# Kernel optimization log

Measured on AMD Instinct MI355X. Metric: run time of the kernel, lower is better.

Reference implementation:

```python
import jax, jax.numpy as jnp
import numpy as np

S = 8192        # packed patch tokens
D = 1024        # hidden_size
H = 16          # num_heads
DH = D // H     # head_dim = 64
N_SEG = 8       # images
SEG = S // N_SEG


def _rope_tables(seq_len, dim, theta=10000.0):
    inv_freq = 1.0 / (theta ** (jnp.arange(0, dim, 2, dtype=jnp.float32) / dim))
    pos = jnp.arange(seq_len, dtype=jnp.float32)
    freqs = pos[:, None] * inv_freq[None, :]          # [S, dim//2]
    emb = jnp.concatenate([freqs, freqs], axis=-1)    # [S, dim]
    return jnp.cos(emb), jnp.sin(emb)


def setup_inputs() -> dict:
    key = jax.random.key(0)
    ks = jax.random.split(key, 6)
    hidden_states = jax.random.normal(ks[0], (S, D), dtype=jnp.float32)
    cu_seqlens = (jnp.arange(N_SEG + 1, dtype=jnp.int32) * SEG)
    cos, sin = _rope_tables(S, DH)
    scale = 1.0 / np.sqrt(D)
    qkv_w = jax.random.normal(ks[1], (3 * D, D), dtype=jnp.float32) * scale
    qkv_b = jax.random.normal(ks[2], (3 * D,), dtype=jnp.float32) * 0.02
    proj_w = jax.random.normal(ks[3], (D, D), dtype=jnp.float32) * scale
    proj_b = jax.random.normal(ks[4], (D,), dtype=jnp.float32) * 0.02
    return {"hidden_states": hidden_states, "cos": cos, "sin": sin,
            "qkv_w": qkv_w, "qkv_b": qkv_b, "proj_w": proj_w, "proj_b": proj_b,
            "cu_seqlens": cu_seqlens}


def _rotate_half(x):
    x1, x2 = jnp.split(x, 2, axis=-1)
    return jnp.concatenate([-x2, x1], axis=-1)


def reference(hidden_states, cos, sin, qkv_w, qkv_b, proj_w, proj_b, cu_seqlens):
    seq = hidden_states.shape[0]
    n_seg = cu_seqlens.shape[0] - 1
    seg = seq // n_seg  # equal-length packed segments

    qkv = hidden_states @ qkv_w.T + qkv_b                # [S, 3D]
    qkv = qkv.reshape(seq, 3, H, DH)
    q, k, v = qkv[:, 0], qkv[:, 1], qkv[:, 2]            # [S, H, DH]

    # rotary in fp32, cos/sin broadcast over heads (unsqueeze(-2))
    cosf = cos[:, None, :].astype(jnp.float32)
    sinf = sin[:, None, :].astype(jnp.float32)
    qf = q.astype(jnp.float32)
    kf = k.astype(jnp.float32)
    q = (qf * cosf + _rotate_half(qf) * sinf).astype(q.dtype)
    k = (kf * cosf + _rotate_half(kf) * sinf).astype(k.dtype)

    # block-diagonal attention over cu_seqlens segments (all equal length)
    qb = q.reshape(n_seg, seg, H, DH)
    kb = k.reshape(n_seg, seg, H, DH)
    vb = v.reshape(n_seg, seg, H, DH)
    scaling = DH ** -0.5
    scores = jnp.einsum('nqhd,nkhd->nhqk', qb, kb) * scaling
    probs = jax.nn.softmax(scores.astype(jnp.float32), axis=-1).astype(qb.dtype)
    out = jnp.einsum('nhqk,nkhd->nqhd', probs, vb)       # [n, seg, H, DH]
    out = out.reshape(seq, D)

    return out @ proj_w.T + proj_b
```

## Files before the change

kernel.cpp:

```cpp
#include <hip/hip_runtime.h>
#include <hip/hip_bf16.h>
#include <cstdint>
#include <cstddef>

typedef __bf16 bf16_t;
typedef __bf16 bf16x4 __attribute__((ext_vector_type(4)));
typedef __bf16 bf16x8 __attribute__((ext_vector_type(8)));
typedef float  f32x4  __attribute__((ext_vector_type(4)));

#define S_LEN 8192
#define NHEAD 16
#define DHEAD 64
#define NSEG  8
#define SEG   1024

#define QSCALE 0.1803368801111204f

__device__ __forceinline__ void stage16(const void* gsrc, void* lds_base, int lane) {
#if __has_builtin(__builtin_amdgcn_global_load_lds)
  (void)lane;
  __builtin_amdgcn_global_load_lds(
      (__attribute__((address_space(1))) void*)(gsrc),
      (__attribute__((address_space(3))) void*)(lds_base), 16, 0, 0);
#else
  ((uint4*)lds_base)[lane] = *(const uint4*)gsrc;
#endif
}

__global__ __launch_bounds__(256) void cvt_tile_kernel(
    const float* __restrict__ s0, bf16_t* __restrict__ d0,
    const float* __restrict__ s1, bf16_t* __restrict__ d1,
    const float* __restrict__ s2, bf16_t* __restrict__ d2) {
  __shared__ __align__(16) bf16_t T[16 * 1024];
  int b = blockIdx.x;
  const float* src; bf16_t* dst; int rb;
  if (b < 512)      { src = s0; dst = d0; rb = b; }
  else if (b < 704) { src = s1; dst = d1; rb = b - 512; }
  else              { src = s2; dst = d2; rb = b - 704; }
  const int t = threadIdx.x;
  const size_t base4 = (size_t)rb * 4096;
#pragma unroll
  for (int i = 0; i < 16; i++) {
    int f = i * 256 + t;
    float4 v = ((const float4*)src)[base4 + f];
    bf16x4 o = {(bf16_t)v.x, (bf16_t)v.y, (bf16_t)v.z, (bf16_t)v.w};
    *(bf16x4*)&T[f * 4] = o;
  }
  __syncthreads();
  bf16_t* dt = dst + (size_t)rb * 16384;
#pragma unroll
  for (int i = 0; i < 8; i++) {
    int o = i * 2048 + t * 8;
    int tile = o >> 9, kb = (o >> 7) & 3, r = (o >> 3) & 15;
    bf16x8 v = *(const bf16x8*)&T[r * 1024 + tile * 32 + kb * 8];
    *(bf16x8*)&dt[o] = v;
  }
}

template<int MODE, int N, int K>
__global__ __launch_bounds__(256, 2) void gemm_bt_kernel(
    const bf16_t* __restrict__ A, const bf16_t* __restrict__ B,
    const float* __restrict__ bias, void* __restrict__ Cout,
    bf16_t* __restrict__ vt, const float* __restrict__ cosT,
    const float* __restrict__ sinT) {
  __shared__ __align__(16) bf16_t As[2][128 * 32];
  __shared__ __align__(16) bf16_t Bs[2][128 * 32];
  const int tid = threadIdx.x;
  const int wv = tid >> 6, lane = tid & 63;
  const int quad = lane >> 4, l16 = lane & 15;
  const int m0 = blockIdx.y * 128, n0 = blockIdx.x * 128;
  const int wm = (wv >> 1) * 64, wn = (wv & 1) * 64;

  constexpr int KT = K / 32;
  const int c0 = wv * 2, c1 = wv * 2 + 1;
  const bf16_t* Ap0 = A + ((size_t)((m0 >> 4) + c0) * KT) * 512 + lane * 8;
  const bf16_t* Ap1 = A + ((size_t)((m0 >> 4) + c1) * KT) * 512 + lane * 8;
  const bf16_t* Bp0 = B + ((size_t)((n0 >> 4) + c0) * KT) * 512 + lane * 8;
  const bf16_t* Bp1 = B + ((size_t)((n0 >> 4) + c1) * KT) * 512 + lane * 8;

  f32x4 acc[4][4];
#pragma unroll
  for (int i = 0; i < 4; i++)
#pragma unroll
    for (int j = 0; j < 4; j++) {
      f32x4 z = {0.f, 0.f, 0.f, 0.f};
      acc[i][j] = z;
    }

  stage16(Ap0, &As[0][c0 * 512], lane);
  stage16(Ap1, &As[0][c1 * 512], lane);
  stage16(Bp0, &Bs[0][c0 * 512], lane);
  stage16(Bp1, &Bs[0][c1 * 512], lane);

  for (int kbi = 0; kbi < KT; kbi++) {
    __syncthreads();
    if (kbi + 1 < KT) {
      const int kb = (kbi + 1) * 512;
      bf16_t* ad = As[(kbi + 1) & 1];
      bf16_t* bd = Bs[(kbi + 1) & 1];
      stage16(Ap0 + kb, ad + c0 * 512, lane);
      stage16(Ap1 + kb, ad + c1 * 512, lane);
      stage16(Bp0 + kb, bd + c0 * 512, lane);
      stage16(Bp1 + kb, bd + c1 * 512, lane);
    }
    const bf16_t* as = As[kbi & 1];
    const bf16_t* bs = Bs[kbi & 1];
    bf16x8 af[4], bfr[4];
#pragma unroll
    for (int i = 0; i < 4; i++)
      af[i] = *(const bf16x8*)&as[((wm >> 4) + i) * 512 + lane * 8];
#pragma unroll
    for (int j = 0; j < 4; j++)
      bfr[j] = *(const bf16x8*)&bs[((wn >> 4) + j) * 512 + lane * 8];
#pragma unroll
    for (int i = 0; i < 4; i++)
#pragma unroll
      for (int j = 0; j < 4; j++)
        acc[i][j] = __builtin_amdgcn_mfma_f32_16x16x32_bf16(af[i], bfr[j], acc[i][j], 0, 0, 0);
  }

#pragma unroll
  for (int i = 0; i < 4; i++) {
    const int row = m0 + wm + i * 16 + quad * 4;
#pragma unroll
    for (int j = 0; j < 4; j++) {
      const int col = n0 + wn + j * 16 + l16;
      if (MODE == 0) {
        if (col < 2048) {
          if (j < 2) {
            bf16_t* qkp = (bf16_t*)Cout;
            const int d = col & 63;
            const float bv0 = bias[col];
            const float bv1 = bias[col + 32];
            const bool isq = (col < 1024);
            const int cb0 = (col >> 3) & 7;
            const int cb1 = cb0 + 4;
            const size_t base = (size_t)(col & ~63);
#pragma unroll
            for (int r = 0; r < 4; r++) {
              const int s = row + r;
              const float c = cosT[s * 64 + d];
              const float sn = sinT[s * 64 + d];
              const float x1 = acc[i][j][r] + bv0;
              const float x2 = acc[i][j + 2][r] + bv1;
              float o1 = x1 * c - x2 * sn;
              float o2 = x2 * c + x1 * sn;
              if (isq) { o1 *= QSCALE; o2 *= QSCALE; }
              const int sw = s & 7;
              const size_t rb = (size_t)s * 2048 + base + (col & 7);
              qkp[rb + ((cb0 ^ sw) * 8)] = (bf16_t)o1;
              qkp[rb + ((cb1 ^ sw) * 8)] = (bf16_t)o2;
            }
          }
        } else {
          const float bv = bias[col];
          const int h = (col - 2048) >> 6, d = (col - 2048) & 63;
          const int seg = row >> 10, kl0 = row & 1023;
          const int blk = (((kl0 & 63) >> 3) ^ (d & 7));
          bf16x4 pk = {(bf16_t)(acc[i][j][0] + bv), (bf16_t)(acc[i][j][1] + bv),
                       (bf16_t)(acc[i][j][2] + bv), (bf16_t)(acc[i][j][3] + bv)};
          *(bf16x4*)&vt[((size_t)((seg * NHEAD + h) * DHEAD + d)) * SEG +
                        (kl0 & ~63) + blk * 8 + (kl0 & 7)] = pk;
        }
      } else {
        const float bv = bias[col];
        float* cp = (float*)Cout;
#pragma unroll
        for (int r = 0; r < 4; r++)
          cp[(size_t)(row + r) * N + col] = acc[i][j][r] + bv;
      }
    }
  }
}

__global__ __launch_bounds__(256, 2) void attn_kernel(
    const bf16_t* __restrict__ qk, const bf16_t* __restrict__ vt,
    bf16_t* __restrict__ attn) {
  __shared__ __align__(16) bf16_t Qs[64 * 64];
  __shared__ __align__(16) bf16_t Ks[2][64 * 64];
  __shared__ __align__(16) bf16_t Vs[2][64 * 64];
  __shared__ __align__(16) bf16_t Ps[4][16 * 64];

  const int bid = blockIdx.x;
  const int qt = bid & 15;
  const int h = (bid >> 4) & 15;
  const int seg = bid >> 8;
  const int tid = threadIdx.x;
  const int wv = tid >> 6, lane = tid & 63;
  const int quad = lane >> 4, l16 = lane & 15;
  const int swl = l16 & 7;

  const int c0 = wv * 2, c1 = c0 + 1;
  const int r8 = lane >> 3;
  const int k8 = (lane & 7) * 8;

  const bf16_t* kbase = qk + 1024 + h * 64;
  const bf16_t* vbase = vt + (size_t)((seg * NHEAD + h) * DHEAD) * SEG;

  {
    size_t rowbase = (size_t)(seg * SEG + qt * 64);
    stage16(qk + (rowbase + c0 * 8 + r8) * 2048 + h * 64 + k8, &Qs[c0 * 512], lane);
    stage16(qk + (rowbase + c1 * 8 + r8) * 2048 + h * 64 + k8, &Qs[c1 * 512], lane);
    size_t krow = (size_t)(seg * SEG);
    stage16(kbase + (krow + c0 * 8 + r8) * 2048 + k8, &Ks[0][c0 * 512], lane);
    stage16(kbase + (krow + c1 * 8 + r8) * 2048 + k8, &Ks[0][c1 * 512], lane);
    stage16(vbase + (size_t)(c0 * 8 + r8) * SEG + k8, &Vs[0][c0 * 512], lane);
    stage16(vbase + (size_t)(c1 * 8 + r8) * SEG + k8, &Vs[0][c1 * 512], lane);
  }
  __syncthreads();
  const bf16x8 aq0 = *(const bf16x8*)&Qs[(wv * 16 + l16) * 64 + (quad ^ swl) * 8];
  const bf16x8 aq1 = *(const bf16x8*)&Qs[(wv * 16 + l16) * 64 + ((quad + 4) ^ swl) * 8];

  float rs[4] = {0.f, 0.f, 0.f, 0.f};
  f32x4 o[4];
#pragma unroll
  for (int jd = 0; jd < 4; jd++) { f32x4 z = {0.f, 0.f, 0.f, 0.f}; o[jd] = z; }

  for (int kt = 0; kt < 16; kt++) {
    __syncthreads();
    if (kt + 1 < 16) {
      const int nb = (kt + 1) & 1;
      size_t krow = (size_t)(seg * SEG + (kt + 1) * 64);
      stage16(kbase + (krow + c0 * 8 + r8) * 2048 + k8, &Ks[nb][c0 * 512], lane);
      stage16(kbase + (krow + c1 * 8 + r8) * 2048 + k8, &Ks[nb][c1 * 512], lane);
      stage16(vbase + (size_t)(c0 * 8 + r8) * SEG + (kt + 1) * 64 + k8, &Vs[nb][c0 * 512], lane);
      stage16(vbase + (size_t)(c1 * 8 + r8) * SEG + (kt + 1) * 64 + k8, &Vs[nb][c1 * 512], lane);
    }
    const bf16_t* ks = Ks[kt & 1];
    const bf16_t* vs = Vs[kt & 1];

    f32x4 sacc[4];
#pragma unroll
    for (int j = 0; j < 4; j++) {
      bf16x8 b0 = *(const bf16x8*)&ks[(j * 16 + l16) * 64 + (quad ^ swl) * 8];
      bf16x8 b1 = *(const bf16x8*)&ks[(j * 16 + l16) * 64 + ((quad + 4) ^ swl) * 8];
      f32x4 s = {0.f, 0.f, 0.f, 0.f};
      s = __builtin_amdgcn_mfma_f32_16x16x32_bf16(aq0, b0, s, 0, 0, 0);
      s = __builtin_amdgcn_mfma_f32_16x16x32_bf16(aq1, b1, s, 0, 0, 0);
      sacc[j] = s;
    }

#pragma unroll
    for (int j = 0; j < 4; j++)
#pragma unroll
      for (int r = 0; r < 4; r++) {
        float e = exp2f(sacc[j][r]);
        rs[r] += e;
        const int prow = quad * 4 + r;
        const int pblk = (j * 2 + (l16 >> 3)) ^ (prow & 7);
        Ps[wv][prow * 64 + pblk * 8 + (l16 & 7)] = (bf16_t)e;
      }

    bf16x8 ap0 = *(const bf16x8*)&Ps[wv][l16 * 64 + (quad ^ swl) * 8];
    bf16x8 ap1 = *(const bf16x8*)&Ps[wv][l16 * 64 + ((quad + 4) ^ swl) * 8];
#pragma unroll
    for (int jd = 0; jd < 4; jd++) {
      bf16x8 b0 = *(const bf16x8*)&vs[(jd * 16 + l16) * 64 + (quad ^ swl) * 8];
      bf16x8 b1 = *(const bf16x8*)&vs[(jd * 16 + l16) * 64 + ((quad + 4) ^ swl) * 8];
      o[jd] = __builtin_amdgcn_mfma_f32_16x16x32_bf16(ap0, b0, o[jd], 0, 0, 0);
      o[jd] = __builtin_amdgcn_mfma_f32_16x16x32_bf16(ap1, b1, o[jd], 0, 0, 0);
    }
  }

#pragma unroll
  for (int r = 0; r < 4; r++) {
#pragma unroll
    for (int off = 1; off < 16; off <<= 1) rs[r] += __shfl_xor(rs[r], off);
    rs[r] = 1.0f / rs[r];
  }

  {
    bf16_t* abase = attn + (size_t)(seg * 64 + qt * 4 + wv) * 16384;
#pragma unroll
    for (int jd = 0; jd < 4; jd++) {
      const int ct = h * 2 + (jd >> 1);
      const int kb = (jd & 1) * 2 + (l16 >> 3);
      const int e = l16 & 7;
#pragma unroll
      for (int r = 0; r < 4; r++)
        abase[ct * 512 + kb * 128 + (quad * 4 + r) * 8 + e] = (bf16_t)(o[jd][r] * rs[r]);
    }
  }
}

extern "C" void kernel_launch(void* const* d_in, const int* in_sizes, int n_in,
                              void* d_out, int out_size, void* d_ws, size_t ws_size,
                              hipStream_t stream) {
  const float* hidden = (const float*)d_in[0];
  const float* cosT   = (const float*)d_in[1];
  const float* sinT   = (const float*)d_in[2];
  const float* qkv_w  = (const float*)d_in[3];
  const float* qkv_b  = (const float*)d_in[4];
  const float* proj_w = (const float*)d_in[5];
  const float* proj_b = (const float*)d_in[6];

  char* ws = (char*)d_ws;
  bf16_t* hs   = (bf16_t*)(ws);
  bf16_t* qw   = (bf16_t*)(ws + 16777216);
  bf16_t* pw   = (bf16_t*)(ws + 23068672);
  bf16_t* qkb  = (bf16_t*)(ws + 25165824);
  bf16_t* vtb  = (bf16_t*)(ws + 58720256);
  bf16_t* attb = (bf16_t*)(ws + 75497472);
  float* out = (float*)d_out;

  cvt_tile_kernel<<<768, 256, 0, stream>>>(hidden, hs, qkv_w, qw, proj_w, pw);

  gemm_bt_kernel<0, 3072, 1024><<<dim3(24, 64), 256, 0, stream>>>(
      hs, qw, qkv_b, (void*)qkb, vtb, cosT, sinT);
  attn_kernel<<<2048, 256, 0, stream>>>(qkb, vtb, attb);
  gemm_bt_kernel<1, 1024, 1024><<<dim3(8, 64), 256, 0, stream>>>(
      attb, pw, proj_b, (void*)out, nullptr, nullptr, nullptr);
}
```

Baseline: 272.2 us.

## Transpose QK^T MFMA to pack P stores, reuse Q LDS, raise occupancy

Swaps the MFMA operand order for the score computation so each lane holds four consecutive key columns of one query row. This lets P be written to LDS as packed bf16x4 stores instead of scalar stores, and turns the row-sum into a single per-lane accumulator reduced with two cross-lane shuffles. The separate P buffer is removed by reusing each wave's Q tile region in LDS, which is safe because Q is already held in registers. Launch bounds rise to 4 blocks per CU, trading register budget for occupancy and adding a shuffle to redistribute the reciprocal sums to the output layout.

```diff
diff --git a/kernel.cpp b/kernel.cpp
--- a/kernel.cpp
+++ b/kernel.cpp
@@ -173,13 +173,12 @@
   }
 }
 
-__global__ __launch_bounds__(256, 2) void attn_kernel(
+__global__ __launch_bounds__(256, 4) void attn_kernel(
     const bf16_t* __restrict__ qk, const bf16_t* __restrict__ vt,
     bf16_t* __restrict__ attn) {
   __shared__ __align__(16) bf16_t Qs[64 * 64];
   __shared__ __align__(16) bf16_t Ks[2][64 * 64];
   __shared__ __align__(16) bf16_t Vs[2][64 * 64];
-  __shared__ __align__(16) bf16_t Ps[4][16 * 64];
 
   const int bid = blockIdx.x;
   const int qt = bid & 15;
@@ -210,8 +209,9 @@
   __syncthreads();
   const bf16x8 aq0 = *(const bf16x8*)&Qs[(wv * 16 + l16) * 64 + (quad ^ swl) * 8];
   const bf16x8 aq1 = *(const bf16x8*)&Qs[(wv * 16 + l16) * 64 + ((quad + 4) ^ swl) * 8];
-
-  float rs[4] = {0.f, 0.f, 0.f, 0.f};
+  bf16_t* Psw = &Qs[wv * 1024];
+
+  float rs = 0.f;
   f32x4 o[4];
 #pragma unroll
   for (int jd = 0; jd < 4; jd++) { f32x4 z = {0.f, 0.f, 0.f, 0.f}; o[jd] = z; }
@@ -235,24 +235,23 @@
       bf16x8 b0 = *(const bf16x8*)&ks[(j * 16 + l16) * 64 + (quad ^ swl) * 8];
       bf16x8 b1 = *(const bf16x8*)&ks[(j * 16 + l16) * 64 + ((quad + 4) ^ swl) * 8];
       f32x4 s = {0.f, 0.f, 0.f, 0.f};
-      s = __builtin_amdgcn_mfma_f32_16x16x32_bf16(aq0, b0, s, 0, 0, 0);
-      s = __builtin_amdgcn_mfma_f32_16x16x32_bf16(aq1, b1, s, 0, 0, 0);
+      s = __builtin_amdgcn_mfma_f32_16x16x32_bf16(b0, aq0, s, 0, 0, 0);
+      s = __builtin_amdgcn_mfma_f32_16x16x32_bf16(b1, aq1, s, 0, 0, 0);
       sacc[j] = s;
     }
 
 #pragma unroll
-    for (int j = 0; j < 4; j++)
-#pragma unroll
-      for (int r = 0; r < 4; r++) {
-        float e = exp2f(sacc[j][r]);
-        rs[r] += e;
-        const int prow = quad * 4 + r;
-        const int pblk = (j * 2 + (l16 >> 3)) ^ (prow & 7);
-        Ps[wv][prow * 64 + pblk * 8 + (l16 & 7)] = (bf16_t)e;
-      }
-
-    bf16x8 ap0 = *(const bf16x8*)&Ps[wv][l16 * 64 + (quad ^ swl) * 8];
-    bf16x8 ap1 = *(const bf16x8*)&Ps[wv][l16 * 64 + ((quad + 4) ^ swl) * 8];
+    for (int j = 0; j < 4; j++) {
+      bf16x4 pk;
+      float e0 = exp2f(sacc[j][0]), e1 = exp2f(sacc[j][1]);
+      float e2 = exp2f(sacc[j][2]), e3 = exp2f(sacc[j][3]);
+      rs += (e0 + e1) + (e2 + e3);
+      pk[0] = (bf16_t)e0; pk[1] = (bf16_t)e1; pk[2] = (bf16_t)e2; pk[3] = (bf16_t)e3;
+      *(bf16x4*)&Psw[l16 * 64 + (((j * 2 + (quad >> 1)) ^ swl) * 8) + (quad & 1) * 4] = pk;
+    }
+
+    bf16x8 ap0 = *(const bf16x8*)&Psw[l16 * 64 + (quad ^ swl) * 8];
+    bf16x8 ap1 = *(const bf16x8*)&Psw[l16 * 64 + ((quad + 4) ^ swl) * 8];
 #pragma unroll
     for (int jd = 0; jd < 4; jd++) {
       bf16x8 b0 = *(const bf16x8*)&vs[(jd * 16 + l16) * 64 + (quad ^ swl) * 8];
@@ -262,12 +261,12 @@
     }
   }
 
-#pragma unroll
-  for (int r = 0; r < 4; r++) {
-#pragma unroll
-    for (int off = 1; off < 16; off <<= 1) rs[r] += __shfl_xor(rs[r], off);
-    rs[r] = 1.0f / rs[r];
-  }
+  rs += __shfl_xor(rs, 16);
+  rs += __shfl_xor(rs, 32);
+  const float rinv = 1.0f / rs;
+  float inv[4];
+#pragma unroll
+  for (int r = 0; r < 4; r++) inv[r] = __shfl(rinv, quad * 20 + r);
 
   {
     bf16_t* abase = attn + (size_t)(seg * 64 + qt * 4 + wv) * 16384;
@@ -278,7 +277,7 @@
       const int e = l16 & 7;
 #pragma unroll
       for (int r = 0; r < 4; r++)
-        abase[ct * 512 + kb * 128 + (quad * 4 + r) * 8 + e] = (bf16_t)(o[jd][r] * rs[r]);
+        abase[ct * 512 + kb * 128 + (quad * 4 + r) * 8 + e] = (bf16_t)(o[jd][r] * inv[r]);
     }
   }
 }
```

Result: faster. 259.9 us (-4.5%).
